# Performance work log

Measured on AMD Instinct MI355X. Metric: run time of the kernel, lower is better.

Reference implementation:

```python
import jax, jax.numpy as jnp
import numpy as np

B, N, D, WIN = 2, 4096, 256, 16


def setup_inputs() -> dict:
    key = jax.random.key(0)
    ks = jax.random.split(key, 10)
    def lin(k, o, i):
        return 0.02 * jax.random.normal(k, (o, i), jnp.float32)
    W = N // WIN
    return {
        "x": 0.5 * jax.random.normal(ks[0], (B, N, D), jnp.float32),
        "embed_qk": jax.random.normal(ks[1], (3, B, W, WIN, WIN, 3), jnp.float32),
        "act_proj_w": lin(ks[2], D, D), "act_proj_b": jnp.zeros((D,), jnp.float32),
        "proj_ln_g": jnp.ones((D,), jnp.float32), "proj_ln_b": jnp.zeros((D,), jnp.float32),
        "conv_w": lin(ks[3], D, D), "conv_b": jnp.zeros((D,), jnp.float32),
        "q_w": lin(ks[4], D, D), "q_b": jnp.zeros((D,), jnp.float32),
        "k_w": lin(ks[5], D, D), "k_b": jnp.zeros((D,), jnp.float32),
        "p_w": lin(ks[6], 1, 3), "p_b": jnp.zeros((1,), jnp.float32),
        "lin_w": lin(ks[7], D, D), "lin_b": jnp.zeros((D,), jnp.float32),
        "norm_g": jnp.ones((D,), jnp.float32), "norm_b": jnp.zeros((D,), jnp.float32),
    }


def _ln(x, g, b, eps=1e-5):
    m = x.mean(-1, keepdims=True)
    v = ((x - m) ** 2).mean(-1, keepdims=True)
    return (x - m) * jax.lax.rsqrt(v + eps) * g + b


def reference(x, embed_qk, act_proj_w, act_proj_b, proj_ln_g, proj_ln_b,
              conv_w, conv_b, q_w, q_b, k_w, k_b, p_w, p_b,
              lin_w, lin_b, norm_g, norm_b):
    # MSMAttentionLayer: gated residual path
    act_res = jax.nn.silu(x @ act_proj_w.T + act_proj_b)          # (B,N,C)
    h = _ln(x, proj_ln_g, proj_ln_b)
    h = jax.nn.silu(h @ conv_w.T + conv_b)                        # 1x1 conv == per-token linear

    # MSMLMultiHeadAttention, stage=1 (window 4x4=16); N % 16 == 0 so add_row_num = 0
    q = jax.nn.elu(h @ q_w.T + q_b) + 1.0
    k = jax.nn.elu(h @ k_w.T + k_b) + 1.0
    v = h
    Bn, Nn, C = h.shape
    Wn = Nn // WIN
    q_win = q.reshape(Bn, Wn, WIN, C)
    k_win = k.reshape(Bn, Wn, WIN, C)
    v_win = v.reshape(Bn, Wn, WIN, C)
    # learned relative-position bias: Linear(3,1) on embed_qk[stage]
    p = (embed_qk[1] @ p_w.T + p_b)[..., 0]
    # second elu+1 feature map (applied on top of q/k which are already elu+1)
    phi_q = jax.nn.elu(q_win) + 1.0
    phi_k = jax.nn.elu(k_win) + 1.0
    # linear-attention style KV aggregation: reduces over windows w
    KV = jnp.einsum('bwmc,bwmd->bmcd', phi_k, v_win)
    att = jnp.einsum('bwnc,bmcd->bwnmd', phi_q, KV) + p[..., None]
    attn_out = att.reshape(Bn, -1, C)[:, :Nn, :]                  # (B,N,C)

    hid = (attn_out * act_res) @ lin_w.T + lin_b
    return _ln(hid + h, norm_g, norm_b)
```

## Files before the change

### kernel.cpp

```cpp
#include <hip/hip_runtime.h>


#define DIM 256
#define NTOK 4096

typedef __attribute__((ext_vector_type(8))) short short8;
typedef __attribute__((ext_vector_type(4))) short short4v;
typedef __attribute__((ext_vector_type(4))) float f32x4;

__device__ __forceinline__ float silu_f(float z) { return z / (1.f + __expf(-z)); }
__device__ __forceinline__ float elu2_f(float z) { return z > 0.f ? z + 2.f : __expf(z) + 1.f; }

__device__ __forceinline__ short f2bf(float f) {
    union { float f; unsigned u; } v; v.f = f;
    unsigned r = v.u + 0x7fffu + ((v.u >> 16) & 1u);
    return (short)(r >> 16);
}
__device__ __forceinline__ float bf2f(short s) {
    union { unsigned u; float f; } v; v.u = ((unsigned)(unsigned short)s) << 16;
    return v.f;
}
__device__ __forceinline__ short8 cvt8(const float* src) {
    const float4 a = *(const float4*)src;
    const float4 c = *(const float4*)(src + 4);
    short8 s;
    s[0] = f2bf(a.x); s[1] = f2bf(a.y); s[2] = f2bf(a.z); s[3] = f2bf(a.w);
    s[4] = f2bf(c.x); s[5] = f2bf(c.y); s[6] = f2bf(c.z); s[7] = f2bf(c.w);
    return s;
}

__global__ __launch_bounds__(256) void fused_dual(
        const float* __restrict__ XF,
        const float* __restrict__ W0f, const float* __restrict__ b0, short* __restrict__ Y0,
        const float* __restrict__ W1f, const float* __restrict__ b1, short* __restrict__ Y1,
        const float* __restrict__ G, const float* __restrict__ Bt) {
    __shared__ __align__(16) short Xs[128 * 72];
    __shared__ __align__(16) short Ws[64 * 72];
    __shared__ float stats[128][2];
    const int zz = blockIdx.z;
    const float* Wf = zz ? W1f : W0f;
    const float* bias = zz ? b1 : b0;
    short* Y = zz ? Y1 : Y0;
    const int tid = threadIdx.x;
    const int wv = tid >> 6, l = tid & 63;
    const int lr = l & 15, lk = l >> 4;
    const int r0 = blockIdx.x * 128, c0 = blockIdx.y * 64;
    const int wm = (wv >> 1) * 64, wn = (wv & 1) * 32;

    if (zz) {
        const int prow = tid >> 1, phalf = tid & 1;
        const float* src = XF + (size_t)(r0 + prow) * DIM + phalf * 128;
        float a1 = 0.f, a2 = 0.f;
        #pragma unroll 8
        for (int j = 0; j < 32; ++j) {
            const float4 v = *(const float4*)(src + j * 4);
            a1 += v.x + v.y + v.z + v.w;
            a2 += v.x * v.x + v.y * v.y + v.z * v.z + v.w * v.w;
        }
        a1 += __shfl_xor(a1, 1);
        a2 += __shfl_xor(a2, 1);
        if (!phalf) {
            const float mm = a1 * (1.f / DIM);
            stats[prow][0] = mm;
            stats[prow][1] = rsqrtf(a2 * (1.f / DIM) - mm * mm + 1e-5f);
        }
        __syncthreads();
    }

    f32x4 acc[4][2];
    #pragma unroll
    for (int i = 0; i < 4; ++i)
        #pragma unroll
        for (int j = 0; j < 2; ++j) acc[i][j] = (f32x4){0.f, 0.f, 0.f, 0.f};
    const int sr = tid >> 3, sc = (tid & 7) * 8;
    for (int kt = 0; kt < DIM; kt += 64) {
        float gv[8], bv[8];
        if (zz) {
            const float4 g1 = *(const float4*)(G + kt + sc);
            const float4 g2 = *(const float4*)(G + kt + sc + 4);
            const float4 t1 = *(const float4*)(Bt + kt + sc);
            const float4 t2 = *(const float4*)(Bt + kt + sc + 4);
            gv[0] = g1.x; gv[1] = g1.y; gv[2] = g1.z; gv[3] = g1.w;
            gv[4] = g2.x; gv[5] = g2.y; gv[6] = g2.z; gv[7] = g2.w;
            bv[0] = t1.x; bv[1] = t1.y; bv[2] = t1.z; bv[3] = t1.w;
            bv[4] = t2.x; bv[5] = t2.y; bv[6] = t2.z; bv[7] = t2.w;
        }
        #pragma unroll
        for (int p = 0; p < 4; ++p) {
            const int row = sr + p * 32;
            const float* src = XF + (size_t)(r0 + row) * DIM + kt + sc;
            const float4 a = *(const float4*)src;
            const float4 c = *(const float4*)(src + 4);
            float v[8] = {a.x, a.y, a.z, a.w, c.x, c.y, c.z, c.w};
            short8 s;
            if (zz) {
                const float mm = stats[row][0], rs = stats[row][1];
                #pragma unroll
                for (int j = 0; j < 8; ++j) s[j] = f2bf((v[j] - mm) * rs * gv[j] + bv[j]);
            } else {
                #pragma unroll
                for (int j = 0; j < 8; ++j) s[j] = f2bf(v[j]);
            }
            *(short8*)&Xs[row * 72 + sc] = s;
        }
        #pragma unroll
        for (int p = 0; p < 2; ++p) {
            const int row = sr + p * 32;
            *(short8*)&Ws[row * 72 + sc] = cvt8(Wf + (size_t)(c0 + row) * DIM + kt + sc);
        }
        __syncthreads();
        #pragma unroll
        for (int kc = 0; kc < 2; ++kc) {
            short8 af[4], bfr[2];
            #pragma unroll
            for (int mi = 0; mi < 4; ++mi)
                af[mi] = *(const short8*)&Xs[(wm + mi * 16 + lr) * 72 + kc * 32 + lk * 8];
            #pragma unroll
            for (int ni = 0; ni < 2; ++ni)
                bfr[ni] = *(const short8*)&Ws[(wn + ni * 16 + lr) * 72 + kc * 32 + lk * 8];
            #pragma unroll
            for (int mi = 0; mi < 4; ++mi)
                #pragma unroll
                for (int ni = 0; ni < 2; ++ni)
                    acc[mi][ni] = __builtin_amdgcn_mfma_f32_16x16x32_bf16(af[mi], bfr[ni], acc[mi][ni], 0, 0, 0);
        }
        __syncthreads();
    }
    #pragma unroll
    for (int mi = 0; mi < 4; ++mi)
        #pragma unroll
        for (int ni = 0; ni < 2; ++ni) {
            const int c = c0 + wn + ni * 16 + lr;
            const float bv2 = bias[c];
            #pragma unroll
            for (int i = 0; i < 4; ++i) {
                const int r = r0 + wm + mi * 16 + lk * 4 + i;
                Y[(size_t)r * DIM + c] = f2bf(silu_f(acc[mi][ni][i] + bv2));
            }
        }
}

__global__ __launch_bounds__(256) void gemm_kq(
        const short* __restrict__ H, const float* __restrict__ Wkf, const float* __restrict__ bk, short* __restrict__ PK,
        const float* __restrict__ Wqf, const float* __restrict__ bq, short* __restrict__ PQ) {
    __shared__ __align__(16) short Xs[128 * 72];
    __shared__ __align__(16) short Ws[64 * 72];
    const int bx = blockIdx.x;
    const bool isq = bx >= 64;
    const float* Wf = isq ? Wqf : Wkf;
    const float* bias = isq ? bq : bk;
    short* Y = isq ? PQ : PK;
    const int r0 = (isq ? bx - 64 : bx) * 128;
    const int c0 = blockIdx.y * 64;
    const int tid = threadIdx.x;
    const int wv = tid >> 6, l = tid & 63;
    const int lr = l & 15, lk = l >> 4;
    const int wm = (wv >> 1) * 64, wn = (wv & 1) * 32;
    f32x4 acc[4][2];
    #pragma unroll
    for (int i = 0; i < 4; ++i)
        #pragma unroll
        for (int j = 0; j < 2; ++j) acc[i][j] = (f32x4){0.f, 0.f, 0.f, 0.f};
    const int sr = tid >> 3, sc = (tid & 7) * 8;
    for (int kt = 0; kt < DIM; kt += 64) {
        #pragma unroll
        for (int p = 0; p < 4; ++p) {
            const int row = sr + p * 32;
            int grow = r0 + row;
            if (isq) grow = ((grow >> 8) << 12) + (grow & 255);
            *(short8*)&Xs[row * 72 + sc] = *(const short8*)(H + (size_t)grow * DIM + kt + sc);
        }
        #pragma unroll
        for (int p = 0; p < 2; ++p) {
            const int row = sr + p * 32;
            *(short8*)&Ws[row * 72 + sc] = cvt8(Wf + (size_t)(c0 + row) * DIM + kt + sc);
        }
        __syncthreads();
        #pragma unroll
        for (int kc = 0; kc < 2; ++kc) {
            short8 af[4], bfr[2];
            #pragma unroll
            for (int mi = 0; mi < 4; ++mi)
                af[mi] = *(const short8*)&Xs[(wm + mi * 16 + lr) * 72 + kc * 32 + lk * 8];
            #pragma unroll
            for (int ni = 0; ni < 2; ++ni)
                bfr[ni] = *(const short8*)&Ws[(wn + ni * 16 + lr) * 72 + kc * 32 + lk * 8];
            #pragma unroll
            for (int mi = 0; mi < 4; ++mi)
                #pragma unroll
                for (int ni = 0; ni < 2; ++ni)
                    acc[mi][ni] = __builtin_amdgcn_mfma_f32_16x16x32_bf16(af[mi], bfr[ni], acc[mi][ni], 0, 0, 0);
        }
        __syncthreads();
    }
    #pragma unroll
    for (int mi = 0; mi < 4; ++mi)
        #pragma unroll
        for (int ni = 0; ni < 2; ++ni) {
            const int c = c0 + wn + ni * 16 + lr;
            const float bv = bias[c];
            #pragma unroll
            for (int i = 0; i < 4; ++i) {
                const int r = r0 + wm + mi * 16 + lk * 4 + i;
                Y[(size_t)r * DIM + c] = f2bf(elu2_f(acc[mi][ni][i] + bv));
            }
        }
}

__global__ __launch_bounds__(256) void kv_mfma(const short* __restrict__ HB, const short* __restrict__ PK,
                                               short* __restrict__ KVT) {
    __shared__ __align__(16) short Hs[64 * 68];
    __shared__ __align__(16) short Ps[64 * 68];
    const int tid = threadIdx.x;
    const int bm = blockIdx.x, b = bm >> 4, m = bm & 15;
    const int d0 = blockIdx.y * 64, c0 = blockIdx.z * 64;
    const int wv = tid >> 6, l = tid & 63;
    const int lr = l & 15, lk = l >> 4;
    const int wd = (wv >> 1) * 32, wc = (wv & 1) * 32;
    f32x4 acc[2][2];
    #pragma unroll
    for (int i = 0; i < 2; ++i)
        #pragma unroll
        for (int j = 0; j < 2; ++j) acc[i][j] = (f32x4){0.f, 0.f, 0.f, 0.f};
    const size_t hbase = (size_t)b * NTOK * DIM;
    const int sr = tid >> 3, sc = (tid & 7) * 8;
    for (int kt = 0; kt < 256; kt += 64) {
        #pragma unroll
        for (int p = 0; p < 2; ++p) {
            const int w = sr + p * 32;
            const size_t gg = hbase + (size_t)((kt + w) * 16 + m) * DIM;
            short8 hv = *(const short8*)(HB + gg + d0 + sc);
            short8 pv = *(const short8*)(PK + gg + c0 + sc);
            *(short4v*)&Hs[w * 68 + sc]     = __builtin_shufflevector(hv, hv, 0, 1, 2, 3);
            *(short4v*)&Hs[w * 68 + sc + 4] = __builtin_shufflevector(hv, hv, 4, 5, 6, 7);
            *(short4v*)&Ps[w * 68 + sc]     = __builtin_shufflevector(pv, pv, 0, 1, 2, 3);
            *(short4v*)&Ps[w * 68 + sc + 4] = __builtin_shufflevector(pv, pv, 4, 5, 6, 7);
        }
        __syncthreads();
        #pragma unroll
        for (int kc = 0; kc < 2; ++kc) {
            const int kb = kc * 32 + lk * 8;
            short8 af[2], bfr[2];
            #pragma unroll
            for (int di = 0; di < 2; ++di)
                #pragma unroll
                for (int i = 0; i < 8; ++i)
                    af[di][i] = Hs[(kb + i) * 68 + wd + di * 16 + lr];
            #pragma unroll
            for (int ci = 0; ci < 2; ++ci)
                #pragma unroll
                for (int i = 0; i < 8; ++i)
                    bfr[ci][i] = Ps[(kb + i) * 68 + wc + ci * 16 + lr];
            #pragma unroll
            for (int di = 0; di < 2; ++di)
                #pragma unroll
                for (int ci = 0; ci < 2; ++ci)
                    acc[di][ci] = __builtin_amdgcn_mfma_f32_16x16x32_bf16(af[di], bfr[ci], acc[di][ci], 0, 0, 0);
        }
        __syncthreads();
    }
    #pragma unroll
    for (int di = 0; di < 2; ++di)
        #pragma unroll
        for (int ci = 0; ci < 2; ++ci)
            #pragma unroll
            for (int i = 0; i < 4; ++i) {
                const int d = d0 + wd + di * 16 + lk * 4 + i;
                const int c = c0 + wc + ci * 16 + lr;
                KVT[((size_t)bm * DIM + d) * DIM + c] = f2bf(acc[di][ci][i]);
            }
}

__global__ __launch_bounds__(256) void attlin(
        const short* __restrict__ PQ, const short* __restrict__ KVT,
        const float* __restrict__ emb, const float* __restrict__ pw, const float* __restrict__ pb,
        const short* __restrict__ AR,
        const float* __restrict__ WLf, const float* __restrict__ bl,
        const short* __restrict__ HB, const float* __restrict__ G, const float* __restrict__ Bt,
        float* __restrict__ Y) {
    __shared__ __align__(16) short Qs[32 * 264];
    __shared__ __align__(16) short AGs[32 * 264];
    __shared__ __align__(16) short Bs[256 * 72];
    __shared__ float s1buf[32][2];
    __shared__ float s2buf[32][2];
    const int tid = threadIdx.x;
    const int wv = tid >> 6, l = tid & 63;
    const int lr = l & 15, lk = l >> 4;
    const int bm = blockIdx.x, b = bm >> 4, m = bm & 15;
    const int q0 = blockIdx.y * 32;
    const int wq = (wv >> 1) * 16;
    const int wd = (wv & 1) * 32;
    const int sr = tid >> 3, sc = (tid & 7) * 8;

    #pragma unroll
    for (int p = 0; p < 4; ++p) {
        const int chunk = tid + p * 256;
        const int row = chunk >> 5, cc = (chunk & 31) * 8;
        *(short8*)&Qs[row * 264 + cc] = *(const short8*)(PQ + (size_t)(b * 256 + q0 + row) * DIM + cc);
    }

    f32x4 accA[4][2];
    #pragma unroll
    for (int i = 0; i < 4; ++i)
        #pragma unroll
        for (int j = 0; j < 2; ++j) accA[i][j] = (f32x4){0.f, 0.f, 0.f, 0.f};
    for (int kt = 0; kt < DIM; kt += 64) {
        #pragma unroll
        for (int p = 0; p < 8; ++p) {
            const int row = sr + p * 32;
            *(short8*)&Bs[row * 72 + sc] = *(const short8*)(KVT + ((size_t)bm * DIM + row) * DIM + kt + sc);
        }
        __syncthreads();
        #pragma unroll
        for (int kc = 0; kc < 2; ++kc) {
            const short8 af = *(const short8*)&Qs[(wq + lr) * 264 + kt + kc * 32 + lk * 8];
            #pragma unroll
            for (int dc = 0; dc < 4; ++dc)
                #pragma unroll
                for (int ni = 0; ni < 2; ++ni) {
                    const short8 bfr = *(const short8*)&Bs[(dc * 64 + wd + ni * 16 + lr) * 72 + kc * 32 + lk * 8];
                    accA[dc][ni] = __builtin_amdgcn_mfma_f32_16x16x32_bf16(af, bfr, accA[dc][ni], 0, 0, 0);
                }
        }
        __syncthreads();
    }
    {
        const float pw0 = pw[0], pw1 = pw[1], pw2 = pw[2], pbv = pb[0];
        #pragma unroll
        for (int i = 0; i < 4; ++i) {
            const int rloc = wq + lk * 4 + i;
            const int qr = q0 + rloc;
            const int widx = qr >> 4, nidx = qr & 15;
            const float* e = emb + ((((size_t)(2 + b) * 256 + widx) * 16 + nidx) * 16 + m) * 3;
            const float pv = e[0] * pw0 + e[1] * pw1 + e[2] * pw2 + pbv;
            const int t = qr * 16 + m;
            #pragma unroll
            for (int dc = 0; dc < 4; ++dc)
                #pragma unroll
                for (int ni = 0; ni < 2; ++ni) {
                    const int d = dc * 64 + wd + ni * 16 + lr;
                    const size_t o = ((size_t)b * NTOK + t) * DIM + d;
                    AGs[rloc * 264 + d] = f2bf((accA[dc][ni][i] + pv) * bf2f(AR[o]));
                }
        }
    }
    __syncthreads();

    const int wn2 = (wv & 1) * 128;
    f32x4 accB[8];
    #pragma unroll
    for (int i = 0; i < 8; ++i) accB[i] = (f32x4){0.f, 0.f, 0.f, 0.f};
    for (int kt = 0; kt < DIM; kt += 64) {
        #pragma unroll
        for (int p = 0; p < 8; ++p) {
            const int row = sr + p * 32;
            *(short8*)&Bs[row * 72 + sc] = cvt8(WLf + (size_t)row * DIM + kt + sc);
        }
        __syncthreads();
        #pragma unroll
        for (int kc = 0; kc < 2; ++kc) {
            const short8 af = *(const short8*)&AGs[(wq + lr) * 264 + kt + kc * 32 + lk * 8];
            #pragma unroll
            for (int ni = 0; ni < 8; ++ni) {
                const short8 bfr = *(const short8*)&Bs[(wn2 + ni * 16 + lr) * 72 + kc * 32 + lk * 8];
                accB[ni] = __builtin_amdgcn_mfma_f32_16x16x32_bf16(af, bfr, accB[ni], 0, 0, 0);
            }
        }
        __syncthreads();
    }
    float s1[4] = {0.f, 0.f, 0.f, 0.f}, s2[4] = {0.f, 0.f, 0.f, 0.f};
    #pragma unroll
    for (int ni = 0; ni < 8; ++ni) {
        const int col = wn2 + ni * 16 + lr;
        const float bv = bl[col];
        #pragma unroll
        for (int i = 0; i < 4; ++i) {
            const int rloc = wq + lk * 4 + i;
            const int t = (q0 + rloc) * 16 + m;
            const float z = accB[ni][i] + bv + bf2f(HB[((size_t)b * NTOK + t) * DIM + col]);
            accB[ni][i] = z;
            s1[i] += z; s2[i] += z * z;
        }
    }
    #pragma unroll
    for (int o = 1; o < 16; o <<= 1) {
        #pragma unroll
        for (int i = 0; i < 4; ++i) {
            s1[i] += __shfl_xor(s1[i], o);
            s2[i] += __shfl_xor(s2[i], o);
        }
    }
    if (lr == 0) {
        #pragma unroll
        for (int i = 0; i < 4; ++i) {
            const int rloc = wq + lk * 4 + i;
            s1buf[rloc][wv & 1] = s1[i];
            s2buf[rloc][wv & 1] = s2[i];
        }
    }
    __syncthreads();
    float mean[4], rstd[4];
    #pragma unroll
    for (int i = 0; i < 4; ++i) {
        const int rloc = wq + lk * 4 + i;
        const float t1 = s1buf[rloc][0] + s1buf[rloc][1];
        const float t2 = s2buf[rloc][0] + s2buf[rloc][1];
        const float mm = t1 * (1.f / DIM);
        mean[i] = mm;
        rstd[i] = rsqrtf(t2 * (1.f / DIM) - mm * mm + 1e-5f);
    }
    #pragma unroll
    for (int ni = 0; ni < 8; ++ni) {
        const int col = wn2 + ni * 16 + lr;
        const float gv = G[col], bv2 = Bt[col];
        #pragma unroll
        for (int i = 0; i < 4; ++i) {
            const int rloc = wq + lk * 4 + i;
            const int t = (q0 + rloc) * 16 + m;
            Y[((size_t)b * NTOK + t) * DIM + col] = (accB[ni][i] - mean[i]) * rstd[i] * gv + bv2;
        }
    }
}

extern "C" void kernel_launch(void* const* d_in, const int* in_sizes, int n_in,
                              void* d_out, int out_size, void* d_ws, size_t ws_size,
                              hipStream_t stream) {
    const float* x   = (const float*)d_in[0];
    const float* emb = (const float*)d_in[1];
    const float* Wa  = (const float*)d_in[2];
    const float* ba  = (const float*)d_in[3];
    const float* lng = (const float*)d_in[4];
    const float* lnb = (const float*)d_in[5];
    const float* Wc  = (const float*)d_in[6];
    const float* bc  = (const float*)d_in[7];
    const float* Wq  = (const float*)d_in[8];
    const float* bq  = (const float*)d_in[9];
    const float* Wk  = (const float*)d_in[10];
    const float* bk  = (const float*)d_in[11];
    const float* pw  = (const float*)d_in[12];
    const float* pb  = (const float*)d_in[13];
    const float* Wl  = (const float*)d_in[14];
    const float* bl  = (const float*)d_in[15];
    const float* ng  = (const float*)d_in[16];
    const float* nb  = (const float*)d_in[17];

    char* ws = (char*)d_ws;
    const size_t MB = 1024 * 1024;
    short* h_bf   = (short*)(ws + 0 * MB);
    short* phik   = (short*)(ws + 4 * MB);
    short* phiq   = (short*)(ws + 8 * MB);
    short* kvT    = (short*)(ws + 9 * MB);
    short* act_bf = (short*)(ws + 13 * MB);

    const dim3 blk(256);
    fused_dual<<<dim3(64, 4, 2), blk, 0, stream>>>(x, Wa, ba, act_bf, Wc, bc, h_bf, lng, lnb);
    gemm_kq<<<dim3(68, 4), blk, 0, stream>>>(h_bf, Wk, bk, phik, Wq, bq, phiq);
    kv_mfma<<<dim3(32, 4, 4), blk, 0, stream>>>(h_bf, phik, kvT);
    attlin<<<dim3(32, 8), blk, 0, stream>>>(phiq, kvT, emb, pw, pb, act_bf, Wl, bl,
                                            h_bf, ng, nb, (float*)d_out);
}
```

Measured before the change: 58.63 us.

## Fuse act/conv projections with K/Q GEMMs into one mega kernel

Merges the dual projection kernel and the K/Q GEMM kernel into a single 512-thread kernel. Each block owns 64 rows across all 256 output columns and keeps the silu'd h tile in shared memory, so the K and Q projections read it from LDS instead of reloading from global memory. This removes one launch and one global round-trip of h. In exchange the grid drops to 256 blocks with large shared-memory use, and only a few blocks do the extra Q GEMM, which may cause load imbalance and lower occupancy.

```diff
diff --git a/kernel.cpp b/kernel.cpp
--- a/kernel.cpp
+++ b/kernel.cpp
@@ -29,37 +29,38 @@
     return s;
 }
 
-__global__ __launch_bounds__(256) void fused_dual(
+__global__ __launch_bounds__(512) void mega(
         const float* __restrict__ XF,
-        const float* __restrict__ W0f, const float* __restrict__ b0, short* __restrict__ Y0,
-        const float* __restrict__ W1f, const float* __restrict__ b1, short* __restrict__ Y1,
+        const float* __restrict__ Waf, const float* __restrict__ ba, short* __restrict__ ACT,
+        const float* __restrict__ Wcf, const float* __restrict__ bc, short* __restrict__ H,
+        const float* __restrict__ Wkf, const float* __restrict__ bk, short* __restrict__ PK,
+        const float* __restrict__ Wqf, const float* __restrict__ bq, short* __restrict__ PQ,
         const float* __restrict__ G, const float* __restrict__ Bt) {
-    __shared__ __align__(16) short Xs[128 * 72];
-    __shared__ __align__(16) short Ws[64 * 72];
-    __shared__ float stats[128][2];
+    __shared__ __align__(16) short Xs[64 * 72];
+    __shared__ __align__(16) short Ws[256 * 72];
+    __shared__ __align__(16) short Hs[64 * 264];
+    __shared__ float stats[64][2];
+    const int tid = threadIdx.x;
     const int zz = blockIdx.z;
-    const float* Wf = zz ? W1f : W0f;
-    const float* bias = zz ? b1 : b0;
-    short* Y = zz ? Y1 : Y0;
-    const int tid = threadIdx.x;
+    const int r0 = blockIdx.x * 64;
     const int wv = tid >> 6, l = tid & 63;
     const int lr = l & 15, lk = l >> 4;
-    const int r0 = blockIdx.x * 128, c0 = blockIdx.y * 64;
-    const int wm = (wv >> 1) * 64, wn = (wv & 1) * 32;
+    const int wm = (wv >> 2) * 32, wn = (wv & 3) * 64;
+    const int sr = tid >> 3, sc = (tid & 7) * 8;
 
     if (zz) {
-        const int prow = tid >> 1, phalf = tid & 1;
-        const float* src = XF + (size_t)(r0 + prow) * DIM + phalf * 128;
+        const int prow = tid >> 3, pseg = tid & 7;
+        const float* src = XF + (size_t)(r0 + prow) * DIM + pseg * 32;
         float a1 = 0.f, a2 = 0.f;
-        #pragma unroll 8
-        for (int j = 0; j < 32; ++j) {
+        #pragma unroll
+        for (int j = 0; j < 8; ++j) {
             const float4 v = *(const float4*)(src + j * 4);
             a1 += v.x + v.y + v.z + v.w;
             a2 += v.x * v.x + v.y * v.y + v.z * v.z + v.w * v.w;
         }
-        a1 += __shfl_xor(a1, 1);
-        a2 += __shfl_xor(a2, 1);
-        if (!phalf) {
+        #pragma unroll
+        for (int o = 1; o < 8; o <<= 1) { a1 += __shfl_xor(a1, o); a2 += __shfl_xor(a2, o); }
+        if (pseg == 0) {
             const float mm = a1 * (1.f / DIM);
             stats[prow][0] = mm;
             stats[prow][1] = rsqrtf(a2 * (1.f / DIM) - mm * mm + 1e-5f);
@@ -67,144 +68,175 @@
         __syncthreads();
     }
 
-    f32x4 acc[4][2];
-    #pragma unroll
-    for (int i = 0; i < 4; ++i)
-        #pragma unroll
-        for (int j = 0; j < 2; ++j) acc[i][j] = (f32x4){0.f, 0.f, 0.f, 0.f};
-    const int sr = tid >> 3, sc = (tid & 7) * 8;
+    const float* Wf1 = zz ? Wcf : Waf;
+    const float* b1 = zz ? bc : ba;
+    f32x4 acc[2][4];
+    #pragma unroll
+    for (int i = 0; i < 2; ++i)
+        #pragma unroll
+        for (int j = 0; j < 4; ++j) acc[i][j] = (f32x4){0.f, 0.f, 0.f, 0.f};
     for (int kt = 0; kt < DIM; kt += 64) {
-        float gv[8], bv[8];
-        if (zz) {
-            const float4 g1 = *(const float4*)(G + kt + sc);
-            const float4 g2 = *(const float4*)(G + kt + sc + 4);
-            const float4 t1 = *(const float4*)(Bt + kt + sc);
-            const float4 t2 = *(const float4*)(Bt + kt + sc + 4);
-            gv[0] = g1.x; gv[1] = g1.y; gv[2] = g1.z; gv[3] = g1.w;
-            gv[4] = g2.x; gv[5] = g2.y; gv[6] = g2.z; gv[7] = g2.w;
-            bv[0] = t1.x; bv[1] = t1.y; bv[2] = t1.z; bv[3] = t1.w;
-            bv[4] = t2.x; bv[5] = t2.y; bv[6] = t2.z; bv[7] = t2.w;
-        }
-        #pragma unroll
-        for (int p = 0; p < 4; ++p) {
-            const int row = sr + p * 32;
-            const float* src = XF + (size_t)(r0 + row) * DIM + kt + sc;
+        {
+            const float* src = XF + (size_t)(r0 + sr) * DIM + kt + sc;
             const float4 a = *(const float4*)src;
             const float4 c = *(const float4*)(src + 4);
             float v[8] = {a.x, a.y, a.z, a.w, c.x, c.y, c.z, c.w};
             short8 s;
             if (zz) {
-                const float mm = stats[row][0], rs = stats[row][1];
+                const float mm = stats[sr][0], rs = stats[sr][1];
+                const float4 g1 = *(const float4*)(G + kt + sc);
+                const float4 g2 = *(const float4*)(G + kt + sc + 4);
+                const float4 t1 = *(const float4*)(Bt + kt + sc);
+                const float4 t2 = *(const float4*)(Bt + kt + sc + 4);
+                const float gv[8] = {g1.x, g1.y, g1.z, g1.w, g2.x, g2.y, g2.z, g2.w};
+                const float bv[8] = {t1.x, t1.y, t1.z, t1.w, t2.x, t2.y, t2.z, t2.w};
                 #pragma unroll
                 for (int j = 0; j < 8; ++j) s[j] = f2bf((v[j] - mm) * rs * gv[j] + bv[j]);
             } else {
                 #pragma unroll
                 for (int j = 0; j < 8; ++j) s[j] = f2bf(v[j]);
             }
-            *(short8*)&Xs[row * 72 + sc] = s;
-        }
-        #pragma unroll
-        for (int p = 0; p < 2; ++p) {
-            const int row = sr + p * 32;
-            *(short8*)&Ws[row * 72 + sc] = cvt8(Wf + (size_t)(c0 + row) * DIM + kt + sc);
+            *(short8*)&Xs[sr * 72 + sc] = s;
+        }
+        #pragma unroll
+        for (int p = 0; p < 4; ++p) {
+            const int row = sr + p * 64;
+            *(short8*)&Ws[row * 72 + sc] = cvt8(Wf1 + (size_t)row * DIM + kt + sc);
         }
         __syncthreads();
         #pragma unroll
         for (int kc = 0; kc < 2; ++kc) {
-            short8 af[4], bfr[2];
-            #pragma unroll
-            for (int mi = 0; mi < 4; ++mi)
+            short8 af[2], bfr[4];
+            #pragma unroll
+            for (int mi = 0; mi < 2; ++mi)
                 af[mi] = *(const short8*)&Xs[(wm + mi * 16 + lr) * 72 + kc * 32 + lk * 8];
             #pragma unroll
-            for (int ni = 0; ni < 2; ++ni)
+            for (int ni = 0; ni < 4; ++ni)
                 bfr[ni] = *(const short8*)&Ws[(wn + ni * 16 + lr) * 72 + kc * 32 + lk * 8];
             #pragma unroll
-            for (int mi = 0; mi < 4; ++mi)
-                #pragma unroll
-                for (int ni = 0; ni < 2; ++ni)
+            for (int mi = 0; mi < 2; ++mi)
+                #pragma unroll
+                for (int ni = 0; ni < 4; ++ni)
                     acc[mi][ni] = __builtin_amdgcn_mfma_f32_16x16x32_bf16(af[mi], bfr[ni], acc[mi][ni], 0, 0, 0);
         }
         __syncthreads();
     }
-    #pragma unroll
-    for (int mi = 0; mi < 4; ++mi)
-        #pragma unroll
-        for (int ni = 0; ni < 2; ++ni) {
-            const int c = c0 + wn + ni * 16 + lr;
-            const float bv2 = bias[c];
+    if (!zz) {
+        #pragma unroll
+        for (int mi = 0; mi < 2; ++mi)
+            #pragma unroll
+            for (int ni = 0; ni < 4; ++ni) {
+                const int col = wn + ni * 16 + lr;
+                const float bv = b1[col];
+                #pragma unroll
+                for (int i = 0; i < 4; ++i) {
+                    const int row = wm + mi * 16 + lk * 4 + i;
+                    ACT[(size_t)(r0 + row) * DIM + col] = f2bf(silu_f(acc[mi][ni][i] + bv));
+                }
+            }
+        return;
+    }
+    #pragma unroll
+    for (int mi = 0; mi < 2; ++mi)
+        #pragma unroll
+        for (int ni = 0; ni < 4; ++ni) {
+            const int col = wn + ni * 16 + lr;
+            const float bv = b1[col];
             #pragma unroll
             for (int i = 0; i < 4; ++i) {
-                const int r = r0 + wm + mi * 16 + lk * 4 + i;
-                Y[(size_t)r * DIM + c] = f2bf(silu_f(acc[mi][ni][i] + bv2));
-            }
-        }
-}
-
-__global__ __launch_bounds__(256) void gemm_kq(
-        const short* __restrict__ H, const float* __restrict__ Wkf, const float* __restrict__ bk, short* __restrict__ PK,
-        const float* __restrict__ Wqf, const float* __restrict__ bq, short* __restrict__ PQ) {
-    __shared__ __align__(16) short Xs[128 * 72];
-    __shared__ __align__(16) short Ws[64 * 72];
-    const int bx = blockIdx.x;
-    const bool isq = bx >= 64;
-    const float* Wf = isq ? Wqf : Wkf;
-    const float* bias = isq ? bq : bk;
-    short* Y = isq ? PQ : PK;
-    const int r0 = (isq ? bx - 64 : bx) * 128;
-    const int c0 = blockIdx.y * 64;
-    const int tid = threadIdx.x;
-    const int wv = tid >> 6, l = tid & 63;
-    const int lr = l & 15, lk = l >> 4;
-    const int wm = (wv >> 1) * 64, wn = (wv & 1) * 32;
-    f32x4 acc[4][2];
-    #pragma unroll
-    for (int i = 0; i < 4; ++i)
-        #pragma unroll
-        for (int j = 0; j < 2; ++j) acc[i][j] = (f32x4){0.f, 0.f, 0.f, 0.f};
-    const int sr = tid >> 3, sc = (tid & 7) * 8;
+                const int row = wm + mi * 16 + lk * 4 + i;
+                const short hv = f2bf(silu_f(acc[mi][ni][i] + bv));
+                H[(size_t)(r0 + row) * DIM + col] = hv;
+                Hs[row * 264 + col] = hv;
+            }
+        }
+    __syncthreads();
+
+    #pragma unroll
+    for (int i = 0; i < 2; ++i)
+        #pragma unroll
+        for (int j = 0; j < 4; ++j) acc[i][j] = (f32x4){0.f, 0.f, 0.f, 0.f};
     for (int kt = 0; kt < DIM; kt += 64) {
         #pragma unroll
         for (int p = 0; p < 4; ++p) {
-            const int row = sr + p * 32;
-            int grow = r0 + row;
-            if (isq) grow = ((grow >> 8) << 12) + (grow & 255);
-            *(short8*)&Xs[row * 72 + sc] = *(const short8*)(H + (size_t)grow * DIM + kt + sc);
-        }
-        #pragma unroll
-        for (int p = 0; p < 2; ++p) {
-            const int row = sr + p * 32;
-            *(short8*)&Ws[row * 72 + sc] = cvt8(Wf + (size_t)(c0 + row) * DIM + kt + sc);
+            const int row = sr + p * 64;
+            *(short8*)&Ws[row * 72 + sc] = cvt8(Wkf + (size_t)row * DIM + kt + sc);
         }
         __syncthreads();
         #pragma unroll
         for (int kc = 0; kc < 2; ++kc) {
-            short8 af[4], bfr[2];
-            #pragma unroll
-            for (int mi = 0; mi < 4; ++mi)
-                af[mi] = *(const short8*)&Xs[(wm + mi * 16 + lr) * 72 + kc * 32 + lk * 8];
-            #pragma unroll
-            for (int ni = 0; ni < 2; ++ni)
+            short8 af[2], bfr[4];
+            #pragma unroll
+            for (int mi = 0; mi < 2; ++mi)
+                af[mi] = *(const short8*)&Hs[(wm + mi * 16 + lr) * 264 + kt + kc * 32 + lk * 8];
+            #pragma unroll
+            for (int ni = 0; ni < 4; ++ni)
                 bfr[ni] = *(const short8*)&Ws[(wn + ni * 16 + lr) * 72 + kc * 32 + lk * 8];
             #pragma unroll
-            for (int mi = 0; mi < 4; ++mi)
-                #pragma unroll
-                for (int ni = 0; ni < 2; ++ni)
+            for (int mi = 0; mi < 2; ++mi)
+                #pragma unroll
+                for (int ni = 0; ni < 4; ++ni)
                     acc[mi][ni] = __builtin_amdgcn_mfma_f32_16x16x32_bf16(af[mi], bfr[ni], acc[mi][ni], 0, 0, 0);
         }
         __syncthreads();
     }
     #pragma unroll
-    for (int mi = 0; mi < 4; ++mi)
-        #pragma unroll
-        for (int ni = 0; ni < 2; ++ni) {
-            const int c = c0 + wn + ni * 16 + lr;
-            const float bv = bias[c];
+    for (int mi = 0; mi < 2; ++mi)
+        #pragma unroll
+        for (int ni = 0; ni < 4; ++ni) {
+            const int col = wn + ni * 16 + lr;
+            const float bv = bk[col];
             #pragma unroll
             for (int i = 0; i < 4; ++i) {
-                const int r = r0 + wm + mi * 16 + lk * 4 + i;
-                Y[(size_t)r * DIM + c] = f2bf(elu2_f(acc[mi][ni][i] + bv));
-            }
-        }
+                const int row = wm + mi * 16 + lk * 4 + i;
+                PK[(size_t)(r0 + row) * DIM + col] = f2bf(elu2_f(acc[mi][ni][i] + bv));
+            }
+        }
+
+    if ((r0 & 4095) < 256) {
+        const int b = r0 >> 12;
+        const size_t qbase = (size_t)b * 256 + (r0 & 4095);
+        #pragma unroll
+        for (int i = 0; i < 2; ++i)
+            #pragma unroll
+            for (int j = 0; j < 4; ++j) acc[i][j] = (f32x4){0.f, 0.f, 0.f, 0.f};
+        for (int kt = 0; kt < DIM; kt += 64) {
+            #pragma unroll
+            for (int p = 0; p < 4; ++p) {
+                const int row = sr + p * 64;
+                *(short8*)&Ws[row * 72 + sc] = cvt8(Wqf + (size_t)row * DIM + kt + sc);
+            }
+            __syncthreads();
+            #pragma unroll
+            for (int kc = 0; kc < 2; ++kc) {
+                short8 af[2], bfr[4];
+                #pragma unroll
+                for (int mi = 0; mi < 2; ++mi)
+                    af[mi] = *(const short8*)&Hs[(wm + mi * 16 + lr) * 264 + kt + kc * 32 + lk * 8];
+                #pragma unroll
+                for (int ni = 0; ni < 4; ++ni)
+                    bfr[ni] = *(const short8*)&Ws[(wn + ni * 16 + lr) * 72 + kc * 32 + lk * 8];
+                #pragma unroll
+                for (int mi = 0; mi < 2; ++mi)
+                    #pragma unroll
+                    for (int ni = 0; ni < 4; ++ni)
+                        acc[mi][ni] = __builtin_amdgcn_mfma_f32_16x16x32_bf16(af[mi], bfr[ni], acc[mi][ni], 0, 0, 0);
+            }
+            __syncthreads();
+        }
+        #pragma unroll
+        for (int mi = 0; mi < 2; ++mi)
+            #pragma unroll
+            for (int ni = 0; ni < 4; ++ni) {
+                const int col = wn + ni * 16 + lr;
+                const float bv = bq[col];
+                #pragma unroll
+                for (int i = 0; i < 4; ++i) {
+                    const int row = wm + mi * 16 + lk * 4 + i;
+                    PQ[(qbase + row) * DIM + col] = f2bf(elu2_f(acc[mi][ni][i] + bv));
+                }
+            }
+    }
 }
 
 __global__ __launch_bounds__(256) void kv_mfma(const short* __restrict__ HB, const short* __restrict__ PK,
@@ -452,10 +484,9 @@
     short* kvT    = (short*)(ws + 9 * MB);
     short* act_bf = (short*)(ws + 13 * MB);
 
-    const dim3 blk(256);
-    fused_dual<<<dim3(64, 4, 2), blk, 0, stream>>>(x, Wa, ba, act_bf, Wc, bc, h_bf, lng, lnb);
-    gemm_kq<<<dim3(68, 4), blk, 0, stream>>>(h_bf, Wk, bk, phik, Wq, bq, phiq);
-    kv_mfma<<<dim3(32, 4, 4), blk, 0, stream>>>(h_bf, phik, kvT);
-    attlin<<<dim3(32, 8), blk, 0, stream>>>(phiq, kvT, emb, pw, pb, act_bf, Wl, bl,
-                                            h_bf, ng, nb, (float*)d_out);
-}
+    mega<<<dim3(128, 1, 2), dim3(512), 0, stream>>>(
+        x, Wa, ba, act_bf, Wc, bc, h_bf, Wk, bk, phik, Wq, bq, phiq, lng, lnb);
+    kv_mfma<<<dim3(32, 4, 4), dim3(256), 0, stream>>>(h_bf, phik, kvT);
+    attlin<<<dim3(32, 8), dim3(256), 0, stream>>>(phiq, kvT, emb, pw, pb, act_bf, Wl, bl,
+                                                  h_bf, ng, nb, (float*)d_out);
+}
```

Measured after the change: 62.19 us. +6.1%, slower.
